# Performance work log

Measured on AMD Instinct MI355X. Metric: run time of the kernel, lower is better.

Reference implementation:

```python
import jax, jax.numpy as jnp
import numpy as np

TEMPERATURE = 0.07
LOSS_CL_WEIGHT = 1.0
EPS = 1e-12  # F.normalize default eps


def setup_inputs() -> dict:
    key = jax.random.key(0)
    k1, k2 = jax.random.split(key)
    N, S, D = 64, 64, 256
    return {
        "proj_z1": jax.random.normal(k1, (N, S, D), dtype=jnp.float32),
        "proj_z2": jax.random.normal(k2, (N, S, D), dtype=jnp.float32),
    }


def _clean_normalize(x, NS, D):
    # flatten -> replace nan/inf with 0 -> L2 normalize rows
    x = x.reshape(NS, D)
    x = jnp.where(jnp.isfinite(x), x, jnp.zeros((), x.dtype))
    norm = jnp.linalg.norm(x, axis=1, keepdims=True)
    return x / jnp.maximum(norm, EPS)


def reference(proj_z1, proj_z2):
    N, S, D = proj_z1.shape
    NS = N * S
    M = 2 * NS
    f1 = _clean_normalize(proj_z1, NS, D)
    f2 = _clean_normalize(proj_z2, NS, D)
    features = jnp.concatenate([f1, f2], axis=0)          # (M, D)
    sim = features @ features.T                            # (M, M)

    idx = jnp.arange(M)
    # positive pair: row i <-> row (i + NS) mod M (eye blocks in label_matrix)
    positives = sim[idx, (idx + NS) % M] / TEMPERATURE     # (M,)
    # CE denominator = all off-diagonal entries (positives + negatives)
    scores = sim / TEMPERATURE
    scores = jnp.where(idx[:, None] == idx[None, :], -jnp.inf, scores)
    lse = jax.nn.logsumexp(scores, axis=1)                 # (M,)
    loss = jnp.mean(lse - positives)
    return LOSS_CL_WEIGHT * loss
```

## Files before the change

kernel.cpp:

```cpp
#include <hip/hip_runtime.h>
#include <stdint.h>

#define NS_ 4096
#define M_  8192
#define D_  256
#define TEMP 0.07f
#define EXP_SCALE 20.61707212818536f
#define LN2 0.6931471805599453f

typedef short bf16x8 __attribute__((ext_vector_type(8)));
typedef float f32x4  __attribute__((ext_vector_type(4)));
typedef unsigned short ushortx4 __attribute__((ext_vector_type(4)));

static __device__ inline unsigned short f2bf(float x) {
    unsigned u = __float_as_uint(x);
    u += 0x7fffu + ((u >> 16) & 1u);
    return (unsigned short)(u >> 16);
}

static __device__ inline float cleanf(float v) {
    return __builtin_isfinite(v) ? v : 0.0f;
}

#define LDS_LOAD16(gp, lp) \
    __builtin_amdgcn_global_load_lds((const __attribute__((address_space(1))) uint32_t*)(gp), \
                                     (__attribute__((address_space(3))) uint32_t*)(lp), 16, 0, 0)

__global__ __launch_bounds__(256) void knorm(const float* __restrict__ z1,
                                             const float* __restrict__ z2,
                                             short* __restrict__ F,
                                             float* __restrict__ pos,
                                             float* __restrict__ denom,
                                             int* __restrict__ cnt,
                                             float* __restrict__ out) {
    const int wave = threadIdx.x >> 6;
    const int t    = threadIdx.x & 63;
    const int i    = blockIdx.x * 4 + wave;
    const float4* p1 = (const float4*)(z1 + (size_t)i * D_);
    const float4* p2 = (const float4*)(z2 + (size_t)i * D_);
    float4 a = p1[t], b = p2[t];
    a.x = cleanf(a.x); a.y = cleanf(a.y); a.z = cleanf(a.z); a.w = cleanf(a.w);
    b.x = cleanf(b.x); b.y = cleanf(b.y); b.z = cleanf(b.z); b.w = cleanf(b.w);

    float s1 = a.x*a.x + a.y*a.y + a.z*a.z + a.w*a.w;
    float s2 = b.x*b.x + b.y*b.y + b.z*b.z + b.w*b.w;
    float dp = a.x*b.x + a.y*b.y + a.z*b.z + a.w*b.w;
    #pragma unroll
    for (int m = 1; m < 64; m <<= 1) {
        s1 += __shfl_xor(s1, m);
        s2 += __shfl_xor(s2, m);
        dp += __shfl_xor(dp, m);
    }
    const float inv1 = 1.0f / fmaxf(sqrtf(s1), 1e-12f);
    const float inv2 = 1.0f / fmaxf(sqrtf(s2), 1e-12f);

    ushortx4 o1, o2;
    o1.x = f2bf(a.x * inv1); o1.y = f2bf(a.y * inv1); o1.z = f2bf(a.z * inv1); o1.w = f2bf(a.w * inv1);
    o2.x = f2bf(b.x * inv2); o2.y = f2bf(b.y * inv2); o2.z = f2bf(b.z * inv2); o2.w = f2bf(b.w * inv2);
    ((ushortx4*)(F + (size_t)i * D_))[t]          = o1;
    ((ushortx4*)(F + (size_t)(i + NS_) * D_))[t]  = o2;

    if (t == 0) pos[i] = dp * inv1 * inv2;
    if (t < 2)  denom[i * 2 + t] = 0.0f;
    if (i == 0 && t < 32) cnt[t] = 0;
    if (i == 0 && t == 0) out[0] = 0.0f;
}

__global__ __launch_bounds__(256, 2) void kgemm(const short* __restrict__ F,
                                                float* __restrict__ denom,
                                                int* __restrict__ cnt,
                                                const float* __restrict__ pos,
                                                float* __restrict__ out) {
    __shared__ short Bl[2][64 * 256];
    __shared__ int lastflag;
    __shared__ float red[4];

    const int rtile = blockIdx.x >> 4;
    const int cq    = blockIdx.x & 15;
    const int R0 = rtile * 256;
    const int C0 = cq * 512;

    const int tid  = threadIdx.x;
    const int lane = tid & 63;
    const int wave = tid >> 6;
    const int c16  = lane & 15;
    const int quad = lane >> 4;
    const int swz  = c16 & 7;

    int goff[8];
    #pragma unroll
    for (int r2 = 0; r2 < 8; ++r2) {
        int c    = tid + r2 * 256;
        int row  = c >> 5;
        int kg   = (c & 31) ^ (row & 7);
        goff[r2] = row * D_ + kg * 8;
    }

    const short* baseA = F + (size_t)R0 * D_;
    const short* baseB = F + (size_t)C0 * D_;

    auto STAGE = [&](const short* g, int buf) {
        short* l = &Bl[buf][0];
        #pragma unroll
        for (int r2 = 0; r2 < 8; ++r2)
            LDS_LOAD16(g + goff[r2], l + (tid + r2 * 256) * 8);
    };

    STAGE(baseA, 0);

    bf16x8 afrag[4][8];
    const int arow_l = wave * 16 + c16;
    #pragma unroll
    for (int ch = 0; ch < 4; ++ch) {
        const short* nxt = (ch < 3) ? (baseA + (size_t)(ch + 1) * 64 * D_) : baseB;
        STAGE(nxt, (ch + 1) & 1);
        asm volatile("s_waitcnt vmcnt(8)" ::: "memory");
        __builtin_amdgcn_s_barrier();
        const short* bp = &Bl[ch & 1][0];
        #pragma unroll
        for (int ks = 0; ks < 8; ++ks)
            afrag[ch][ks] = *(const bf16x8*)(bp + arow_l * 256 +
                                             (((ks * 4 + quad) ^ (arow_l & 7)) * 8));
        asm volatile("s_waitcnt lgkmcnt(0)" ::: "memory");
        __builtin_amdgcn_s_barrier();
    }

    float accexp[4][4];
    #pragma unroll
    for (int s = 0; s < 4; ++s)
        #pragma unroll
        for (int r = 0; r < 4; ++r) accexp[s][r] = 0.0f;

    for (int it = 0; it < 8; ++it) {
        if (it < 7) {
            STAGE(baseB + (size_t)(it + 1) * 64 * D_, (it + 1) & 1);
            asm volatile("s_waitcnt vmcnt(8)" ::: "memory");
        } else {
            asm volatile("s_waitcnt vmcnt(0)" ::: "memory");
        }
        __builtin_amdgcn_s_barrier();
        const short* bp = &Bl[it & 1][0];

        #pragma unroll
        for (int sub = 0; sub < 4; ++sub) {
            const int tc = sub * 16 + c16;
            bf16x8 bfrag[8];
            #pragma unroll
            for (int ks = 0; ks < 8; ++ks)
                bfrag[ks] = *(const bf16x8*)(bp + tc * 256 +
                                             (((ks * 4 + quad) ^ swz) * 8));
            f32x4 acc[4];
            #pragma unroll
            for (int s = 0; s < 4; ++s) acc[s] = (f32x4){0.f, 0.f, 0.f, 0.f};
            __builtin_amdgcn_s_setprio(1);
            #pragma unroll
            for (int ks = 0; ks < 8; ++ks)
                #pragma unroll
                for (int s = 0; s < 4; ++s)
                    acc[s] = __builtin_amdgcn_mfma_f32_16x16x32_bf16(
                        afrag[s][ks], bfrag[ks], acc[s], 0, 0, 0);
            __builtin_amdgcn_s_setprio(0);

            const int colbase = C0 + it * 64 + sub * 16;
            #pragma unroll
            for (int s = 0; s < 4; ++s) {
                const int rowbase = R0 + s * 64 + wave * 16;
                if (colbase != rowbase) {
                    #pragma unroll
                    for (int r = 0; r < 4; ++r)
                        accexp[s][r] += __builtin_amdgcn_exp2f(acc[s][r] * EXP_SCALE);
                } else {
                    #pragma unroll
                    for (int r = 0; r < 4; ++r) {
                        float e = __builtin_amdgcn_exp2f(acc[s][r] * EXP_SCALE);
                        if (c16 == quad * 4 + r) e = 0.0f;
                        accexp[s][r] += e;
                    }
                }
            }
        }
        asm volatile("s_waitcnt lgkmcnt(0)" ::: "memory");
        __builtin_amdgcn_s_barrier();
    }

    #pragma unroll
    for (int s = 0; s < 4; ++s)
        #pragma unroll
        for (int r = 0; r < 4; ++r) {
            float v = accexp[s][r];
            v += __shfl_xor(v, 1);
            v += __shfl_xor(v, 2);
            v += __shfl_xor(v, 4);
            v += __shfl_xor(v, 8);
            if (c16 == 0)
                atomicAdd(&denom[R0 + s * 64 + wave * 16 + quad * 4 + r], v);
        }

    __syncthreads();
    if (tid == 0) {
        __threadfence();
        lastflag = (atomicAdd(&cnt[rtile], 1) == 15);
    }
    __syncthreads();
    if (lastflag) {
        __threadfence();
        float v = atomicAdd(&denom[R0 + tid], 0.0f);
        float p = __builtin_amdgcn_logf(v) * (LN2 / (float)M_);
        #pragma unroll
        for (int m = 1; m < 64; m <<= 1) p += __shfl_xor(p, m);
        if (lane == 0) red[wave] = p;
        __syncthreads();
        if (tid == 0) atomicAdd(out, red[0] + red[1] + red[2] + red[3]);
        if (rtile == 0) {
            __syncthreads();
            float sp = 0.0f;
            for (int i = tid; i < NS_; i += 256) sp += pos[i];
            #pragma unroll
            for (int m = 1; m < 64; m <<= 1) sp += __shfl_xor(sp, m);
            if (lane == 0) red[wave] = sp;
            __syncthreads();
            if (tid == 0)
                atomicAdd(out, (red[0] + red[1] + red[2] + red[3]) *
                               (-2.0f / (TEMP * (float)M_)));
        }
    }
}

extern "C" void kernel_launch(void* const* d_in, const int* in_sizes, int n_in,
                              void* d_out, int out_size, void* d_ws, size_t ws_size,
                              hipStream_t stream) {
    const float* z1 = (const float*)d_in[0];
    const float* z2 = (const float*)d_in[1];

    short* F     = (short*)d_ws;
    float* denom = (float*)((char*)d_ws + (size_t)M_ * D_ * 2);
    int*   cnt   = (int*)(denom + M_);
    float* pos   = (float*)(cnt + 32);
    float* out   = (float*)d_out;

    knorm<<<NS_ / 4, 256, 0, stream>>>(z1, z2, F, pos, denom, cnt, out);
    kgemm<<<512, 256, 0, stream>>>(F, denom, cnt, pos, out);
}
```

Before: 114.6 us.

## Use 512-thread blocks with triple-buffered LDS and interleaved B-tile prefetch

The GEMM-exp kernel moves from 512 blocks of 256 threads to 256 blocks of 512 threads, each covering 256 rows by 1024 columns. Each wave now holds 32 A rows instead of 64, which halves its A fragment registers. B tiles go through a three-buffer LDS ring, and the next-next tile's loads are issued inside the sub-tile loop, which drops the trailing lgkmcnt wait and barrier from every iteration. The cost is fewer blocks (256 on a chip with about 256 CUs, one block each) and more LDS per block.

```diff
diff --git a/kernel.cpp b/kernel.cpp
--- a/kernel.cpp
+++ b/kernel.cpp
@@ -66,19 +66,19 @@
     if (i == 0 && t == 0) out[0] = 0.0f;
 }
 
-__global__ __launch_bounds__(256, 2) void kgemm(const short* __restrict__ F,
+__global__ __launch_bounds__(512, 1) void kgemm(const short* __restrict__ F,
                                                 float* __restrict__ denom,
                                                 int* __restrict__ cnt,
                                                 const float* __restrict__ pos,
                                                 float* __restrict__ out) {
-    __shared__ short Bl[2][64 * 256];
+    __shared__ short Bl[3][64 * 256];
     __shared__ int lastflag;
-    __shared__ float red[4];
-
-    const int rtile = blockIdx.x >> 4;
-    const int cq    = blockIdx.x & 15;
+    __shared__ float red[8];
+
+    const int rtile = blockIdx.x >> 3;
+    const int cq    = blockIdx.x & 7;
     const int R0 = rtile * 256;
-    const int C0 = cq * 512;
+    const int C0 = cq * 1024;
 
     const int tid  = threadIdx.x;
     const int lane = tid & 63;
@@ -87,59 +87,76 @@
     const int quad = lane >> 4;
     const int swz  = c16 & 7;
 
-    int goff[8];
-    #pragma unroll
-    for (int r2 = 0; r2 < 8; ++r2) {
-        int c    = tid + r2 * 256;
-        int row  = c >> 5;
-        int kg   = (c & 31) ^ (row & 7);
+    int goff[4];
+    #pragma unroll
+    for (int r2 = 0; r2 < 4; ++r2) {
+        int g   = tid + r2 * 512;
+        int row = g >> 5;
+        int kg  = (g & 31) ^ (row & 7);
         goff[r2] = row * D_ + kg * 8;
     }
 
     const short* baseA = F + (size_t)R0 * D_;
     const short* baseB = F + (size_t)C0 * D_;
 
-    auto STAGE = [&](const short* g, int buf) {
-        short* l = &Bl[buf][0];
-        #pragma unroll
-        for (int r2 = 0; r2 < 8; ++r2)
-            LDS_LOAD16(g + goff[r2], l + (tid + r2 * 256) * 8);
-    };
-
-    STAGE(baseA, 0);
-
-    bf16x8 afrag[4][8];
-    const int arow_l = wave * 16 + c16;
+    short* const bufs0 = &Bl[0][0];
+    short* const bufs1 = &Bl[1][0];
+    short* const bufs2 = &Bl[2][0];
+
+    bf16x8 afrag[2][8];
+    const int mych = wave >> 1;
+    const int lrb  = (wave & 1) * 32;
+
+    {
+        #pragma unroll
+        for (int r2 = 0; r2 < 4; ++r2)
+            LDS_LOAD16(baseA + goff[r2], bufs0 + (tid + r2 * 512) * 8);
+    }
     #pragma unroll
     for (int ch = 0; ch < 4; ++ch) {
         const short* nxt = (ch < 3) ? (baseA + (size_t)(ch + 1) * 64 * D_) : baseB;
-        STAGE(nxt, (ch + 1) & 1);
-        asm volatile("s_waitcnt vmcnt(8)" ::: "memory");
+        short* dst = (ch == 0) ? bufs1 : (ch == 1) ? bufs2 : (ch == 2) ? bufs0 : bufs1;
+        #pragma unroll
+        for (int r2 = 0; r2 < 4; ++r2)
+            LDS_LOAD16(nxt + goff[r2], dst + (tid + r2 * 512) * 8);
+        asm volatile("s_waitcnt vmcnt(4)" ::: "memory");
         __builtin_amdgcn_s_barrier();
-        const short* bp = &Bl[ch & 1][0];
-        #pragma unroll
-        for (int ks = 0; ks < 8; ++ks)
-            afrag[ch][ks] = *(const bf16x8*)(bp + arow_l * 256 +
-                                             (((ks * 4 + quad) ^ (arow_l & 7)) * 8));
+        if (mych == ch) {
+            const short* bp = (ch == 0) ? bufs0 : (ch == 1) ? bufs1 : (ch == 2) ? bufs2 : bufs0;
+            #pragma unroll
+            for (int st = 0; st < 2; ++st) {
+                const int row = lrb + st * 16 + c16;
+                #pragma unroll
+                for (int ks = 0; ks < 8; ++ks)
+                    afrag[st][ks] = *(const bf16x8*)(bp + row * 256 +
+                                                     (((ks * 4 + quad) ^ swz) * 8));
+            }
+        }
         asm volatile("s_waitcnt lgkmcnt(0)" ::: "memory");
         __builtin_amdgcn_s_barrier();
     }
-
-    float accexp[4][4];
-    #pragma unroll
-    for (int s = 0; s < 4; ++s)
-        #pragma unroll
-        for (int r = 0; r < 4; ++r) accexp[s][r] = 0.0f;
-
-    for (int it = 0; it < 8; ++it) {
-        if (it < 7) {
-            STAGE(baseB + (size_t)(it + 1) * 64 * D_, (it + 1) & 1);
-            asm volatile("s_waitcnt vmcnt(8)" ::: "memory");
-        } else {
-            asm volatile("s_waitcnt vmcnt(0)" ::: "memory");
-        }
+    {
+        const short* gb = baseB + (size_t)64 * D_;
+        #pragma unroll
+        for (int r2 = 0; r2 < 4; ++r2)
+            LDS_LOAD16(gb + goff[r2], bufs2 + (tid + r2 * 512) * 8);
+    }
+
+    float accexp[2][4];
+    #pragma unroll
+    for (int st = 0; st < 2; ++st)
+        #pragma unroll
+        for (int r = 0; r < 4; ++r) accexp[st][r] = 0.0f;
+
+    short* pr = bufs1;
+    short* pn = bufs2;
+    short* ps = bufs0;
+
+    for (int t = 0; t < 16; ++t) {
+        if (t < 15) { asm volatile("s_waitcnt vmcnt(4)" ::: "memory"); }
+        else        { asm volatile("s_waitcnt vmcnt(0)" ::: "memory"); }
         __builtin_amdgcn_s_barrier();
-        const short* bp = &Bl[it & 1][0];
+        const short* gb2 = baseB + (size_t)(t + 2) * 64 * D_;
 
         #pragma unroll
         for (int sub = 0; sub < 4; ++sub) {
@@ -147,80 +164,86 @@
             bf16x8 bfrag[8];
             #pragma unroll
             for (int ks = 0; ks < 8; ++ks)
-                bfrag[ks] = *(const bf16x8*)(bp + tc * 256 +
+                bfrag[ks] = *(const bf16x8*)(pr + tc * 256 +
                                              (((ks * 4 + quad) ^ swz) * 8));
-            f32x4 acc[4];
-            #pragma unroll
-            for (int s = 0; s < 4; ++s) acc[s] = (f32x4){0.f, 0.f, 0.f, 0.f};
+            if (t < 14)
+                LDS_LOAD16(gb2 + goff[sub], ps + (tid + sub * 512) * 8);
+
+            f32x4 acc0 = (f32x4){0.f, 0.f, 0.f, 0.f};
+            f32x4 acc1 = (f32x4){0.f, 0.f, 0.f, 0.f};
             __builtin_amdgcn_s_setprio(1);
             #pragma unroll
-            for (int ks = 0; ks < 8; ++ks)
-                #pragma unroll
-                for (int s = 0; s < 4; ++s)
-                    acc[s] = __builtin_amdgcn_mfma_f32_16x16x32_bf16(
-                        afrag[s][ks], bfrag[ks], acc[s], 0, 0, 0);
+            for (int ks = 0; ks < 8; ++ks) {
+                acc0 = __builtin_amdgcn_mfma_f32_16x16x32_bf16(afrag[0][ks], bfrag[ks], acc0, 0, 0, 0);
+                acc1 = __builtin_amdgcn_mfma_f32_16x16x32_bf16(afrag[1][ks], bfrag[ks], acc1, 0, 0, 0);
+            }
             __builtin_amdgcn_s_setprio(0);
 
-            const int colbase = C0 + it * 64 + sub * 16;
-            #pragma unroll
-            for (int s = 0; s < 4; ++s) {
-                const int rowbase = R0 + s * 64 + wave * 16;
+            const int colbase = C0 + t * 64 + sub * 16;
+            #pragma unroll
+            for (int st = 0; st < 2; ++st) {
+                const f32x4 acc = st ? acc1 : acc0;
+                const int rowbase = R0 + wave * 32 + st * 16;
                 if (colbase != rowbase) {
                     #pragma unroll
                     for (int r = 0; r < 4; ++r)
-                        accexp[s][r] += __builtin_amdgcn_exp2f(acc[s][r] * EXP_SCALE);
+                        accexp[st][r] += __builtin_amdgcn_exp2f(acc[r] * EXP_SCALE);
                 } else {
                     #pragma unroll
                     for (int r = 0; r < 4; ++r) {
-                        float e = __builtin_amdgcn_exp2f(acc[s][r] * EXP_SCALE);
+                        float e = __builtin_amdgcn_exp2f(acc[r] * EXP_SCALE);
                         if (c16 == quad * 4 + r) e = 0.0f;
-                        accexp[s][r] += e;
+                        accexp[st][r] += e;
                     }
                 }
             }
         }
-        asm volatile("s_waitcnt lgkmcnt(0)" ::: "memory");
-        __builtin_amdgcn_s_barrier();
-    }
-
-    #pragma unroll
-    for (int s = 0; s < 4; ++s)
+        short* tmp = pr; pr = pn; pn = ps; ps = tmp;
+    }
+
+    #pragma unroll
+    for (int st = 0; st < 2; ++st)
         #pragma unroll
         for (int r = 0; r < 4; ++r) {
-            float v = accexp[s][r];
+            float v = accexp[st][r];
             v += __shfl_xor(v, 1);
             v += __shfl_xor(v, 2);
             v += __shfl_xor(v, 4);
             v += __shfl_xor(v, 8);
             if (c16 == 0)
-                atomicAdd(&denom[R0 + s * 64 + wave * 16 + quad * 4 + r], v);
+                atomicAdd(&denom[R0 + wave * 32 + st * 16 + quad * 4 + r], v);
         }
 
     __syncthreads();
     if (tid == 0) {
         __threadfence();
-        lastflag = (atomicAdd(&cnt[rtile], 1) == 15);
+        lastflag = (atomicAdd(&cnt[rtile], 1) == 7);
     }
     __syncthreads();
     if (lastflag) {
         __threadfence();
-        float v = atomicAdd(&denom[R0 + tid], 0.0f);
-        float p = __builtin_amdgcn_logf(v) * (LN2 / (float)M_);
+        float p = 0.0f;
+        if (tid < 256) {
+            float v = atomicAdd(&denom[R0 + tid], 0.0f);
+            p = __builtin_amdgcn_logf(v) * (LN2 / (float)M_);
+        }
         #pragma unroll
         for (int m = 1; m < 64; m <<= 1) p += __shfl_xor(p, m);
         if (lane == 0) red[wave] = p;
         __syncthreads();
-        if (tid == 0) atomicAdd(out, red[0] + red[1] + red[2] + red[3]);
+        if (tid == 0) atomicAdd(out, red[0] + red[1] + red[2] + red[3] +
+                                     red[4] + red[5] + red[6] + red[7]);
         if (rtile == 0) {
             __syncthreads();
             float sp = 0.0f;
-            for (int i = tid; i < NS_; i += 256) sp += pos[i];
+            for (int i = tid; i < NS_; i += 512) sp += pos[i];
             #pragma unroll
             for (int m = 1; m < 64; m <<= 1) sp += __shfl_xor(sp, m);
             if (lane == 0) red[wave] = sp;
             __syncthreads();
             if (tid == 0)
-                atomicAdd(out, (red[0] + red[1] + red[2] + red[3]) *
+                atomicAdd(out, (red[0] + red[1] + red[2] + red[3] +
+                                red[4] + red[5] + red[6] + red[7]) *
                                (-2.0f / (TEMP * (float)M_)));
         }
     }
@@ -239,5 +262,5 @@
     float* out   = (float*)d_out;
 
     knorm<<<NS_ / 4, 256, 0, stream>>>(z1, z2, F, pos, denom, cnt, out);
-    kgemm<<<512, 256, 0, stream>>>(F, denom, cnt, pos, out);
-}
+    kgemm<<<256, 512, 0, stream>>>(F, denom, cnt, pos, out);
+}
```

Result: faster. 111.4 us (-2.8%).
